# Performance work log

Hardware: AMD Instinct MI355X
Metric: run time of the kernel (lower is better)

Reference implementation:

```python
import jax, jax.numpy as jnp
import numpy as np

DIM = 192
NUM_HEADS = 8
EPS = 1e-12  # torch F.normalize default eps


def setup_inputs() -> dict:
    key = jax.random.key(0)
    k1, k2, k3, k4 = jax.random.split(key, 4)
    b, c, h, w = 8, DIM, 128, 128
    x = jax.random.normal(k1, (b, c, h, w), dtype=jnp.float32)
    # 1x1 qkv conv weight, stored as (3c, c)
    w_qkv = jax.random.normal(k2, (3 * c, c), dtype=jnp.float32) * (1.0 / np.sqrt(c))
    # depthwise 3x3 conv weight, groups = 3c -> OIHW (3c, 1, 3, 3)
    w_dw = jax.random.normal(k3, (3 * c, 1, 3, 3), dtype=jnp.float32) * (1.0 / 3.0)
    # 1x1 project_out weight (c, c)
    w_out = jax.random.normal(k4, (c, c), dtype=jnp.float32) * (1.0 / np.sqrt(c))
    temperature = jnp.ones((NUM_HEADS, 1, 1), dtype=jnp.float32)
    return {"x": x, "w_qkv": w_qkv, "w_dw": w_dw, "w_out": w_out,
            "temperature": temperature}


def _mdta(x, w_qkv, w_dw, w_out, temperature):
    b, c, h, w = x.shape
    nh = NUM_HEADS
    # 1x1 conv == channel GEMM
    qkv = jnp.einsum('oc,bchw->bohw', w_qkv, x)
    # depthwise 3x3 conv, groups = 3c
    qkv = jax.lax.conv_general_dilated(
        qkv, w_dw, window_strides=(1, 1), padding='SAME',
        feature_group_count=3 * c,
        dimension_numbers=('NCHW', 'OIHW', 'NCHW'))
    q, k, v = jnp.split(qkv, 3, axis=1)
    hd = c // nh
    q = q.reshape(b, nh, hd, h * w)
    k = k.reshape(b, nh, hd, h * w)
    v = v.reshape(b, nh, hd, h * w)
    # L2 normalize over spatial (hw) dim
    q = q / jnp.maximum(jnp.linalg.norm(q, axis=-1, keepdims=True), EPS)
    k = k / jnp.maximum(jnp.linalg.norm(k, axis=-1, keepdims=True), EPS)
    # channel x channel attention per head: (b, nh, hd, hd)
    attn = jnp.einsum('bhcn,bhdn->bhcd', q, k) * temperature
    attn = jax.nn.softmax(attn, axis=-1)
    out = jnp.einsum('bhcd,bhdn->bhcn', attn, v).reshape(b, c, h, w)
    return jnp.einsum('oc,bchw->bohw', w_out, out)


def reference(x, w_qkv, w_dw, w_out, temperature):
    return _mdta(x, w_qkv, w_dw, w_out, temperature)
```

## Files before the change

### kernel.cpp

```cpp
#include <hip/hip_runtime.h>


#define HW 16384
#define WIMG 128
#define C 192
#define C3 576
#define NH 8
#define HD 24

typedef unsigned short ushort8_t __attribute__((ext_vector_type(8)));
typedef short short8_t __attribute__((ext_vector_type(8)));
typedef float float4_t __attribute__((ext_vector_type(4)));

__device__ __forceinline__ float bfu2f(unsigned short u) {
    union { unsigned int i; float f; } v; v.i = ((unsigned int)u) << 16; return v.f;
}
__device__ __forceinline__ unsigned short f2bfu(float f) {
    union { float f; unsigned int i; } v; v.f = f;
    unsigned int x = v.i;
    return (unsigned short)((x + 0x7FFFu + ((x >> 16) & 1u)) >> 16);
}
__device__ __forceinline__ float inload(const void* p, int idx, int isbf) {
    return isbf ? bfu2f(((const unsigned short*)p)[idx]) : ((const float*)p)[idx];
}

__device__ __forceinline__ int afrag_idx(int o, int dg) {
    return ((((o >> 4) * 6 + (dg >> 5)) * 4 + ((dg >> 3) & 3)) << 7)
           + ((o & 15) << 3) + (dg & 7);
}

__global__ void probe_dtype(const unsigned int* __restrict__ x, int* __restrict__ flag) {
    const int t = threadIdx.x;
    int cnt = 0;
    for (int i = t; i < 512; i += 256) {
        const unsigned int u = x[i] & 0xFFFFu;
        const unsigned int e = (u >> 7) & 0xFFu;
        if (u == 0u || (e >= 100u && e <= 140u)) cnt++;
    }
#pragma unroll
    for (int off = 32; off; off >>= 1) cnt += __shfl_down(cnt, off, 64);
    __shared__ int s[4];
    if ((t & 63) == 0) s[t >> 6] = cnt;
    __syncthreads();
    if (t == 0) flag[0] = (s[0] + s[1] + s[2] + s[3] > 300) ? 1 : 0;
}

__global__ void prep(const void* __restrict__ wqkv, const void* __restrict__ wdw,
                     const void* __restrict__ wout, const void* __restrict__ temp,
                     const int* __restrict__ flagp, unsigned short* __restrict__ wqb,
                     float* __restrict__ wdwf, float* __restrict__ woutf,
                     float* __restrict__ tempf, float* __restrict__ Sraw,
                     float* __restrict__ normsum) {
    const int isbf = flagp[0];
    const int id = blockIdx.x * 256 + threadIdx.x;
    const int stride = gridDim.x * 256;
    for (int i = id; i < C3 * C; i += stride) {
        const int o = i / C, dg = i - o * C;
        const unsigned short v =
            isbf ? ((const unsigned short*)wqkv)[i] : f2bfu(((const float*)wqkv)[i]);
        wqb[afrag_idx(o, dg)] = v;
    }
    for (int i = id; i < C3 * 9; i += stride) wdwf[i] = inload(wdw, i, isbf);
    for (int i = id; i < C * C; i += stride) woutf[i] = inload(wout, i, isbf);
    for (int i = id; i < NH; i += stride) tempf[i] = inload(temp, i, isbf);
    for (int i = id; i < 8 * NH * HD * HD; i += stride) Sraw[i] = 0.f;
    for (int i = id; i < 8 * 2 * C; i += stride) normsum[i] = 0.f;
}

__global__ __launch_bounds__(512) void gemm_mfma(
    const void* __restrict__ Bsrc, const unsigned short* __restrict__ Abf,
    void* __restrict__ outp, const int* __restrict__ flagp,
    size_t b_batch_stride, size_t b_const_off, size_t o_batch_stride,
    int a_batch_stride, int m_tiles, int b_mode, int out_mode) {
    __shared__ unsigned short sbuf[16384];
    const int isbf = flagp[0];
    const int b_isbf = b_mode | isbf;
    const int tid = threadIdx.x;
    const int batch = blockIdx.y;
    const int n0 = blockIdx.x * 128;
    const size_t b_off = b_batch_stride * batch + b_const_off;
    const size_t o_off = o_batch_stride * batch;
    const unsigned short* Ab = Abf + (size_t)a_batch_stride * batch;

    const int w = tid >> 6;
    const int lane = tid & 63;
    const int l15 = lane & 15;
    const int quad = lane >> 4;
    const int mhalf = w & 1;
    const int nquad = w >> 1;

    short8_t bfr[6][2];
#pragma unroll
    for (int h = 0; h < 2; h++) {
        if (h) __syncthreads();
        if (tid < 192) {
            const int cg = tid >> 4;
            const int pg = tid & 15;
            const int chbase = h * 96 + cg * 8;
            ushort8_t rows[8];
            if (b_isbf) {
                const unsigned short* bp = (const unsigned short*)Bsrc + b_off + n0 + pg * 8;
#pragma unroll
                for (int r = 0; r < 8; r++)
                    rows[r] = *reinterpret_cast<const ushort8_t*>(bp + (size_t)(chbase + r) * HW);
            } else {
                const float* bp = (const float*)Bsrc + b_off + n0 + pg * 8;
#pragma unroll
                for (int r = 0; r < 8; r++) {
                    const float4_t f0 = *reinterpret_cast<const float4_t*>(bp + (size_t)(chbase + r) * HW);
                    const float4_t f1 = *reinterpret_cast<const float4_t*>(bp + (size_t)(chbase + r) * HW + 4);
#pragma unroll
                    for (int i = 0; i < 4; i++) { rows[r][i] = f2bfu(f0[i]); rows[r][i + 4] = f2bfu(f1[i]); }
                }
            }
#pragma unroll
            for (int s = 0; s < 8; s++) {
                ushort8_t outv;
#pragma unroll
                for (int r = 0; r < 8; r++) outv[r] = rows[r][s];
                const int p = pg * 8 + s;
                const int cidx = p * 16 + (cg ^ s);
                *reinterpret_cast<ushort8_t*>(&sbuf[cidx * 8]) = outv;
            }
        }
        __syncthreads();
#pragma unroll
        for (int ksl = 0; ksl < 3; ksl++) {
            const int ks = h * 3 + ksl;
            const int cgl = ks * 4 + quad - h * 12;
#pragma unroll
            for (int nt = 0; nt < 2; nt++) {
                const int p = nquad * 32 + nt * 16 + l15;
                const int cidx = p * 16 + (cgl ^ (p & 7));
                bfr[ks][nt] = *reinterpret_cast<const short8_t*>(&sbuf[cidx * 8]);
            }
        }
    }

    const int o_isbf = out_mode ? isbf : 1;
    const int rr = tid >> 3;
    const int kk = tid & 7;
    for (int mt0 = 0; mt0 < m_tiles; mt0++) {
        const int m0 = mt0 * 64;
        short8_t afr[2][6];
#pragma unroll
        for (int mt = 0; mt < 2; mt++) {
            const int tile = mt0 * 4 + mhalf * 2 + mt;
#pragma unroll
            for (int ks = 0; ks < 6; ks++)
                afr[mt][ks] = *reinterpret_cast<const short8_t*>(
                    Ab + (size_t)((((tile * 6 + ks) << 2) + quad) << 7) + (l15 << 3));
        }
        float4_t acc[2][2];
#pragma unroll
        for (int mt = 0; mt < 2; mt++)
#pragma unroll
            for (int nt = 0; nt < 2; nt++) {
                float4_t z = {0.f, 0.f, 0.f, 0.f};
                acc[mt][nt] = z;
            }
#pragma unroll
        for (int ks = 0; ks < 6; ks++)
#pragma unroll
            for (int mt = 0; mt < 2; mt++)
#pragma unroll
                for (int nt = 0; nt < 2; nt++)
                    acc[mt][nt] = __builtin_amdgcn_mfma_f32_16x16x32_bf16(
                        afr[mt][ks], bfr[ks][nt], acc[mt][nt], 0, 0, 0);
        if (o_isbf) {
            __syncthreads();
#pragma unroll
            for (int mt = 0; mt < 2; mt++) {
                const int row64 = (mhalf * 2 + mt) * 16 + quad * 4;
#pragma unroll
                for (int nt = 0; nt < 2; nt++) {
                    const int col = nquad * 32 + nt * 16 + l15;
#pragma unroll
                    for (int r = 0; r < 4; r++)
                        sbuf[(row64 + r) * 136 + col] = f2bfu(acc[mt][nt][r]);
                }
            }
            __syncthreads();
            const ushort8_t v0 = *reinterpret_cast<const ushort8_t*>(&sbuf[rr * 136 + kk * 16]);
            const ushort8_t v1 = *reinterpret_cast<const ushort8_t*>(&sbuf[rr * 136 + kk * 16 + 8]);
            unsigned short* op = (unsigned short*)outp + o_off + (size_t)(m0 + rr) * HW + n0 + kk * 16;
            *reinterpret_cast<ushort8_t*>(op) = v0;
            *reinterpret_cast<ushort8_t*>(op + 8) = v1;
        } else {
#pragma unroll
            for (int mt = 0; mt < 2; mt++) {
                const int row = m0 + (mhalf * 2 + mt) * 16 + quad * 4;
#pragma unroll
                for (int nt = 0; nt < 2; nt++) {
                    const int col = n0 + nquad * 32 + nt * 16 + l15;
#pragma unroll
                    for (int r = 0; r < 4; r++)
                        ((float*)outp)[o_off + (size_t)(row + r) * HW + col] = acc[mt][nt][r];
                }
            }
        }
    }
}

__global__ void dwconv(const unsigned short* __restrict__ qkv0,
                       const float* __restrict__ wdwf,
                       unsigned short* __restrict__ qkv1,
                       float* __restrict__ normsum) {
    const int ch = blockIdx.y;
    const size_t base = (size_t)blockIdx.z * C3 * HW + (size_t)ch * HW;
    const unsigned short* ip = qkv0 + base;
    const float* wp = wdwf + ch * 9;
    const int p = blockIdx.x * 2048 + threadIdx.x * 8;
    const int y = p >> 7, x0 = p & 127;
    float acc[8];
#pragma unroll
    for (int j = 0; j < 8; j++) acc[j] = 0.f;
#pragma unroll
    for (int dy = 0; dy < 3; dy++) {
        const int yy = y + dy - 1;
        if (yy < 0 || yy > 127) continue;
        const int rb = yy * WIMG + x0;
        const ushort8_t mid = *reinterpret_cast<const ushort8_t*>(ip + rb);
        float f[10];
        f[0] = (x0 > 0) ? bfu2f(ip[rb - 1]) : 0.f;
        f[9] = (x0 < 120) ? bfu2f(ip[rb + 8]) : 0.f;
#pragma unroll
        for (int i = 0; i < 8; i++) f[i + 1] = bfu2f(mid[i]);
        const float w0 = wp[dy * 3], w1 = wp[dy * 3 + 1], w2 = wp[dy * 3 + 2];
#pragma unroll
        for (int j = 0; j < 8; j++) acc[j] += w0 * f[j] + w1 * f[j + 1] + w2 * f[j + 2];
    }
    ushort8_t outv;
#pragma unroll
    for (int j = 0; j < 8; j++) outv[j] = f2bfu(acc[j]);
    *reinterpret_cast<ushort8_t*>(qkv1 + base + p) = outv;

    if (ch < 2 * C) {
        float ss = 0.f;
#pragma unroll
        for (int j = 0; j < 8; j++) ss += acc[j] * acc[j];
#pragma unroll
        for (int off = 32; off; off >>= 1) ss += __shfl_down(ss, off, 64);
        __shared__ float red[4];
        if ((threadIdx.x & 63) == 0) red[threadIdx.x >> 6] = ss;
        __syncthreads();
        if (threadIdx.x == 0)
            atomicAdd(&normsum[blockIdx.z * 2 * C + ch],
                      red[0] + red[1] + red[2] + red[3]);
    }
}

__global__ __launch_bounds__(256) void attn_gram(
    const unsigned short* __restrict__ qkv1, float* __restrict__ Sraw) {
    const int b = blockIdx.z, h = blockIdx.y;
    const int wave = threadIdx.x >> 6;
    const int lane = threadIdx.x & 63;
    const int l15 = lane & 15, quad = lane >> 4;
    const int k0 = (blockIdx.x * 4 + wave) * 512;
    const unsigned short* qrow = qkv1 + (size_t)b * C3 * HW + (size_t)(h * HD) * HW;
    const unsigned short* krow = qkv1 + (size_t)b * C3 * HW + (size_t)(C + h * HD) * HW;

    float4_t acc[2][2];
#pragma unroll
    for (int mt = 0; mt < 2; mt++)
#pragma unroll
        for (int nt = 0; nt < 2; nt++) {
            float4_t z = {0.f, 0.f, 0.f, 0.f};
            acc[mt][nt] = z;
        }

#pragma unroll 4
    for (int ks = 0; ks < 16; ks++) {
        const int kk = k0 + ks * 32 + quad * 8;
        short8_t qa[2], kb[2];
        qa[0] = *reinterpret_cast<const short8_t*>(qrow + (size_t)l15 * HW + kk);
        qa[1] = *reinterpret_cast<const short8_t*>(qrow + (size_t)(16 + l15) * HW + kk);
        kb[0] = *reinterpret_cast<const short8_t*>(krow + (size_t)l15 * HW + kk);
        kb[1] = *reinterpret_cast<const short8_t*>(krow + (size_t)(16 + l15) * HW + kk);
#pragma unroll
        for (int mt = 0; mt < 2; mt++)
#pragma unroll
            for (int nt = 0; nt < 2; nt++)
                acc[mt][nt] = __builtin_amdgcn_mfma_f32_16x16x32_bf16(
                    qa[mt], kb[nt], acc[mt][nt], 0, 0, 0);
    }

    float* Sb = Sraw + (size_t)b * NH * HD * HD + (size_t)h * HD * HD;
#pragma unroll
    for (int nt = 0; nt < 2; nt++) {
        const int j = nt * 16 + l15;
        if (j >= HD) continue;
#pragma unroll
        for (int mt = 0; mt < 2; mt++) {
            const int i0 = mt * 16 + quad * 4;
#pragma unroll
            for (int r = 0; r < 4; r++) {
                const int i = i0 + r;
                if (i < HD) atomicAdd(&Sb[i * HD + j], acc[mt][nt][r]);
            }
        }
    }
}

__global__ void buildM(const float* __restrict__ Sraw, const float* __restrict__ normsum,
                       const float* __restrict__ tempf, const float* __restrict__ woutf,
                       unsigned short* __restrict__ Mb) {
    __shared__ float As[NH * HD * HD];
    __shared__ float inv[2 * C];
    const int b = blockIdx.y;
    const int tid = threadIdx.x;
    for (int r = tid; r < 2 * C; r += 256)
        inv[r] = 1.f / fmaxf(sqrtf(normsum[b * 2 * C + r]), 1e-12f);
    __syncthreads();
    for (int e = tid; e < NH * HD * HD; e += 256) {
        const int h = e / (HD * HD);
        const int rm = e - h * HD * HD;
        const int i = rm / HD, j = rm % HD;
        As[e] = Sraw[(size_t)b * NH * HD * HD + e] * inv[h * HD + i] * inv[C + h * HD + j] * tempf[h];
    }
    __syncthreads();
    if (tid < C) {
        const int h = tid / HD, i = tid % HD;
        float* rp = As + h * HD * HD + i * HD;
        float mx = -1e30f;
#pragma unroll
        for (int j = 0; j < HD; j++) mx = fmaxf(mx, rp[j]);
        float sum = 0.f;
#pragma unroll
        for (int j = 0; j < HD; j++) { rp[j] = __expf(rp[j] - mx); sum += rp[j]; }
        const float is = 1.f / sum;
#pragma unroll
        for (int j = 0; j < HD; j++) rp[j] *= is;
    }
    __syncthreads();
    const int idx = blockIdx.x * 256 + tid;
    const int o = idx / C, dg = idx % C;
    const int h = dg / HD, d = dg % HD;
    const float* wp = woutf + o * C + h * HD;
    const float* Ap = As + h * HD * HD + d;
    float acc = 0.f;
#pragma unroll
    for (int c2 = 0; c2 < HD; c2++) acc += wp[c2] * Ap[c2 * HD];
    Mb[(size_t)b * C * C + afrag_idx(o, dg)] = f2bfu(acc);
}

extern "C" void kernel_launch(void* const* d_in, const int* in_sizes, int n_in,
                              void* d_out, int out_size, void* d_ws, size_t ws_size,
                              hipStream_t stream) {
    const void* x    = d_in[0];
    const void* wqkv = d_in[1];
    const void* wdw  = d_in[2];
    const void* wout = d_in[3];
    const void* temp = d_in[4];

    char* w = (char*)d_ws;
    int* flag = (int*)w;                          w += 64;
    unsigned short* wqb = (unsigned short*)w;     w += (size_t)C3 * C * 2;
    unsigned short* Mb  = (unsigned short*)w;     w += (size_t)8 * C * C * 2;
    float* wdwf  = (float*)w;                     w += (size_t)C3 * 9 * 4;
    float* woutf = (float*)w;                     w += (size_t)C * C * 4;
    float* tempf = (float*)w;                     w += 64;
    float* normsum = (float*)w;                   w += (size_t)8 * 2 * C * 4;
    float* Sraw  = (float*)w;                     w += (size_t)8 * NH * HD * HD * 4;
    unsigned short* qkv0 = (unsigned short*)w;    w += (size_t)8 * C3 * HW * 2;
    unsigned short* qkv1 = (unsigned short*)w;

    probe_dtype<<<1, 256, 0, stream>>>((const unsigned int*)x, flag);
    prep<<<432, 256, 0, stream>>>(wqkv, wdw, wout, temp, flag, wqb, wdwf, woutf,
                                  tempf, Sraw, normsum);
    gemm_mfma<<<dim3(HW / 128, 8), 512, 0, stream>>>(
        x, wqb, qkv0, flag, (size_t)C * HW, 0, (size_t)C3 * HW, 0, 9, 0, 0);
    dwconv<<<dim3(8, C3, 8), 256, 0, stream>>>(qkv0, wdwf, qkv1, normsum);
    attn_gram<<<dim3(8, NH, 8), 256, 0, stream>>>(qkv1, Sraw);
    buildM<<<dim3(144, 8), 256, 0, stream>>>(Sraw, normsum, tempf, woutf, Mb);
    gemm_mfma<<<dim3(HW / 128, 8), 512, 0, stream>>>(
        qkv1, Mb, d_out, flag, (size_t)C3 * HW, (size_t)2 * C * HW, (size_t)C * HW,
        C * C, 3, 1, 1);
}
```

Before: 382.0 us.

## Interleave qkv channels in groups of four and batch dwconv over four channels

The first GEMM now writes its bf16 output in a layout where each group of four channels is interleaved per pixel. Each lane stores its four accumulator rows as one 8-byte vector, with no LDS staging or barriers. The depthwise conv is rewritten to read that layout, so each thread handles four channels with vector loads. Its weights are cached in shared memory and its norm atomics are issued per wave instead of through a block reduction. The risk is that the interleaved layout changes coalescing on both sides, and the larger per-thread register footprint may lower occupancy.

```diff
diff --git a/kernel.cpp b/kernel.cpp
--- a/kernel.cpp
+++ b/kernel.cpp
@@ -9,6 +9,7 @@
 #define HD 24
 
 typedef unsigned short ushort8_t __attribute__((ext_vector_type(8)));
+typedef unsigned short ushort4_t __attribute__((ext_vector_type(4)));
 typedef short short8_t __attribute__((ext_vector_type(8)));
 typedef float float4_t __attribute__((ext_vector_type(4)));
 
@@ -167,7 +168,21 @@
                 for (int nt = 0; nt < 2; nt++)
                     acc[mt][nt] = __builtin_amdgcn_mfma_f32_16x16x32_bf16(
                         afr[mt][ks], bfr[ks][nt], acc[mt][nt], 0, 0, 0);
-        if (o_isbf) {
+        if (out_mode == 0) {
+#pragma unroll
+            for (int mt = 0; mt < 2; mt++) {
+                const int ch4 = (m0 >> 2) + (mhalf * 2 + mt) * 4 + quad;
+#pragma unroll
+                for (int nt = 0; nt < 2; nt++) {
+                    const int px = n0 + nquad * 32 + nt * 16 + l15;
+                    ushort4_t v;
+#pragma unroll
+                    for (int r = 0; r < 4; r++) v[r] = f2bfu(acc[mt][nt][r]);
+                    *reinterpret_cast<ushort4_t*>(
+                        (unsigned short*)outp + o_off + ((size_t)ch4 * HW + px) * 4) = v;
+                }
+            }
+        } else if (o_isbf) {
             __syncthreads();
 #pragma unroll
             for (int mt = 0; mt < 2; mt++) {
@@ -202,51 +217,90 @@
     }
 }
 
-__global__ void dwconv(const unsigned short* __restrict__ qkv0,
-                       const float* __restrict__ wdwf,
-                       unsigned short* __restrict__ qkv1,
-                       float* __restrict__ normsum) {
-    const int ch = blockIdx.y;
-    const size_t base = (size_t)blockIdx.z * C3 * HW + (size_t)ch * HW;
-    const unsigned short* ip = qkv0 + base;
-    const float* wp = wdwf + ch * 9;
+__global__ __launch_bounds__(256) void dwconv(
+    const unsigned short* __restrict__ qkv0i, const float* __restrict__ wdwf,
+    unsigned short* __restrict__ qkv1, float* __restrict__ normsum) {
+    const int cg4 = blockIdx.y;
+    const int b = blockIdx.z;
+    const size_t ibase = ((size_t)b * 144 + cg4) * HW * 4;
+    __shared__ float wsm[36];
+    if (threadIdx.x < 36) wsm[threadIdx.x] = wdwf[cg4 * 36 + threadIdx.x];
+    __syncthreads();
     const int p = blockIdx.x * 2048 + threadIdx.x * 8;
     const int y = p >> 7, x0 = p & 127;
-    float acc[8];
-#pragma unroll
-    for (int j = 0; j < 8; j++) acc[j] = 0.f;
+    float acc[4][8];
+#pragma unroll
+    for (int r = 0; r < 4; r++)
+#pragma unroll
+        for (int j = 0; j < 8; j++) acc[r][j] = 0.f;
 #pragma unroll
     for (int dy = 0; dy < 3; dy++) {
         const int yy = y + dy - 1;
         if (yy < 0 || yy > 127) continue;
         const int rb = yy * WIMG + x0;
-        const ushort8_t mid = *reinterpret_cast<const ushort8_t*>(ip + rb);
-        float f[10];
-        f[0] = (x0 > 0) ? bfu2f(ip[rb - 1]) : 0.f;
-        f[9] = (x0 < 120) ? bfu2f(ip[rb + 8]) : 0.f;
-#pragma unroll
-        for (int i = 0; i < 8; i++) f[i + 1] = bfu2f(mid[i]);
-        const float w0 = wp[dy * 3], w1 = wp[dy * 3 + 1], w2 = wp[dy * 3 + 2];
-#pragma unroll
-        for (int j = 0; j < 8; j++) acc[j] += w0 * f[j] + w1 * f[j + 1] + w2 * f[j + 2];
-    }
-    ushort8_t outv;
-#pragma unroll
-    for (int j = 0; j < 8; j++) outv[j] = f2bfu(acc[j]);
-    *reinterpret_cast<ushort8_t*>(qkv1 + base + p) = outv;
-
-    if (ch < 2 * C) {
-        float ss = 0.f;
-#pragma unroll
-        for (int j = 0; j < 8; j++) ss += acc[j] * acc[j];
-#pragma unroll
-        for (int off = 32; off; off >>= 1) ss += __shfl_down(ss, off, 64);
-        __shared__ float red[4];
-        if ((threadIdx.x & 63) == 0) red[threadIdx.x >> 6] = ss;
-        __syncthreads();
-        if (threadIdx.x == 0)
-            atomicAdd(&normsum[blockIdx.z * 2 * C + ch],
-                      red[0] + red[1] + red[2] + red[3]);
+        float f[4][10];
+#pragma unroll
+        for (int m = 0; m < 4; m++) {
+            const ushort8_t mm =
+                *reinterpret_cast<const ushort8_t*>(qkv0i + ibase + (size_t)(rb + 2 * m) * 4);
+#pragma unroll
+            for (int r = 0; r < 4; r++) {
+                f[r][1 + 2 * m] = bfu2f(mm[r]);
+                f[r][2 + 2 * m] = bfu2f(mm[4 + r]);
+            }
+        }
+        if (x0 > 0) {
+            const ushort4_t el =
+                *reinterpret_cast<const ushort4_t*>(qkv0i + ibase + (size_t)(rb - 1) * 4);
+#pragma unroll
+            for (int r = 0; r < 4; r++) f[r][0] = bfu2f(el[r]);
+        } else {
+#pragma unroll
+            for (int r = 0; r < 4; r++) f[r][0] = 0.f;
+        }
+        if (x0 < 120) {
+            const ushort4_t er =
+                *reinterpret_cast<const ushort4_t*>(qkv0i + ibase + (size_t)(rb + 8) * 4);
+#pragma unroll
+            for (int r = 0; r < 4; r++) f[r][9] = bfu2f(er[r]);
+        } else {
+#pragma unroll
+            for (int r = 0; r < 4; r++) f[r][9] = 0.f;
+        }
+#pragma unroll
+        for (int r = 0; r < 4; r++) {
+            const float w0 = wsm[r * 9 + dy * 3], w1 = wsm[r * 9 + dy * 3 + 1],
+                        w2 = wsm[r * 9 + dy * 3 + 2];
+#pragma unroll
+            for (int j = 0; j < 8; j++)
+                acc[r][j] += w0 * f[r][j] + w1 * f[r][j + 1] + w2 * f[r][j + 2];
+        }
+    }
+#pragma unroll
+    for (int r = 0; r < 4; r++) {
+        ushort8_t outv;
+#pragma unroll
+        for (int j = 0; j < 8; j++) outv[j] = f2bfu(acc[r][j]);
+        *reinterpret_cast<ushort8_t*>(
+            qkv1 + ((size_t)b * C3 + cg4 * 4 + r) * HW + p) = outv;
+    }
+    if (cg4 < 96) {
+        float ss[4];
+#pragma unroll
+        for (int r = 0; r < 4; r++) {
+            float s = 0.f;
+#pragma unroll
+            for (int j = 0; j < 8; j++) s += acc[r][j] * acc[r][j];
+            ss[r] = s;
+        }
+#pragma unroll
+        for (int off = 32; off; off >>= 1)
+#pragma unroll
+            for (int r = 0; r < 4; r++) ss[r] += __shfl_down(ss[r], off, 64);
+        if ((threadIdx.x & 63) == 0)
+#pragma unroll
+            for (int r = 0; r < 4; r++)
+                atomicAdd(&normsum[b * 2 * C + cg4 * 4 + r], ss[r]);
     }
 }
 
@@ -370,7 +424,7 @@
                                   tempf, Sraw, normsum);
     gemm_mfma<<<dim3(HW / 128, 8), 512, 0, stream>>>(
         x, wqb, qkv0, flag, (size_t)C * HW, 0, (size_t)C3 * HW, 0, 9, 0, 0);
-    dwconv<<<dim3(8, C3, 8), 256, 0, stream>>>(qkv0, wdwf, qkv1, normsum);
+    dwconv<<<dim3(8, 144, 8), 256, 0, stream>>>(qkv0, wdwf, qkv1, normsum);
     attn_gram<<<dim3(8, NH, 8), 256, 0, stream>>>(qkv1, Sraw);
     buildM<<<dim3(144, 8), 256, 0, stream>>>(Sraw, normsum, tempf, woutf, Mb);
     gemm_mfma<<<dim3(HW / 128, 8), 512, 0, stream>>>(
```

New measurement: 392.0 us. 2.6% more time.
